# Optimization experiments

Hardware: AMD Instinct MI355X
Metric: run time of the kernel (lower is better)

Reference implementation:

```python
import jax, jax.numpy as jnp
import numpy as np

N_LEVELS = 8
N_FEATS = 8            # features per level
BASE_RES = 16
PER_LEVEL_SCALE = 1.2599210739135742
LOG2_HASHMAP = 19
TABLE_PAD = 8192       # padded per-level table rows (>= max level size 6568)
N_POINTS = 262144


def _level_params(l):
    # tcnn: scale = base * s^l - 1 ; res = ceil(scale)+1 ; size = min(2^19, round_up(res^2, 8))
    scale = BASE_RES * (PER_LEVEL_SCALE ** l) - 1.0
    res = int(np.ceil(scale)) + 1
    size = min(1 << LOG2_HASHMAP, ((res * res + 7) // 8) * 8)
    return float(scale), res, size


def hashgrid_encode(x, table):
    """x: [N,2] in [0,1), table: [L, TABLE_PAD, F]. Returns [N, L*F]."""
    outs = []
    for l in range(N_LEVELS):
        scale, res, size = _level_params(l)
        pos = x * jnp.float32(scale) + jnp.float32(0.5)
        pg = jnp.floor(pos)
        frac = pos - pg
        pg = pg.astype(jnp.int32)
        # Smoothstep interpolation weights: t^2 (3 - 2t)
        w = frac * frac * (3.0 - 2.0 * frac)          # [N,2]
        feat = jnp.zeros((x.shape[0], N_FEATS), dtype=table.dtype)
        for dx in (0, 1):
            wx = w[:, 0] if dx else 1.0 - w[:, 0]
            for dy in (0, 1):
                wy = w[:, 1] if dy else 1.0 - w[:, 1]
                # dense grid index (all levels here fit the hashmap), modulo level size as in tcnn
                idx = ((pg[:, 0] + dx) + (pg[:, 1] + dy) * res) % size
                feat = feat + (wx * wy)[:, None] * table[l, idx]  # irregular gather
        outs.append(feat)
    return jnp.concatenate(outs, axis=-1)  # [N, 64]


def mlp(enc, W0, W1, W2, W3):
    h = jax.nn.relu(enc @ W0)
    h = jax.nn.relu(h @ W1)
    h = jax.nn.relu(h @ W2)
    return h @ W3  # linear output activation


def setup_inputs() -> dict:
    key = jax.random.key(0)
    ks = jax.random.split(key, 6)
    x = jax.random.uniform(ks[0], (N_POINTS, 2), dtype=jnp.float32)
    # tcnn initializes grid params ~ uniform(-1e-4, 1e-4); small values
    table = jax.random.normal(ks[1], (N_LEVELS, TABLE_PAD, N_FEATS), dtype=jnp.float32) * 1e-2
    W0 = jax.random.normal(ks[2], (64, 256), dtype=jnp.float32) * (1.0 / np.sqrt(64))
    W1 = jax.random.normal(ks[3], (256, 256), dtype=jnp.float32) * (1.0 / np.sqrt(256))
    W2 = jax.random.normal(ks[4], (256, 256), dtype=jnp.float32) * (1.0 / np.sqrt(256))
    W3 = jax.random.normal(ks[5], (256, 1), dtype=jnp.float32) * (1.0 / np.sqrt(256))
    return {"x": x, "table": table, "W0": W0, "W1": W1, "W2": W2, "W3": W3}


def reference(x, table, W0, W1, W2, W3):
    enc = hashgrid_encode(x, table)
    return mlp(enc, W0, W1, W2, W3)  # [N, 1]
```

## Files before the change

kernel.cpp:

```cpp
#include <hip/hip_runtime.h>
#include <cmath>


#define N_LEVELS 8
#define TABLE_PAD 8192
#define TILE_M 64
#define ACT_STRIDE 264

typedef __attribute__((ext_vector_type(8))) short short8;
typedef __attribute__((ext_vector_type(16))) float float16v;

struct LevelParams {
  float scale[N_LEVELS];
  int   res[N_LEVELS];
  int   size[N_LEVELS];
};

__device__ __forceinline__ unsigned short f2bf(float f) {
  unsigned int u = __float_as_uint(f);
  u += 0x7fffu + ((u >> 16) & 1u);
  return (unsigned short)(u >> 16);
}
__device__ __forceinline__ unsigned int pack2bf(float a, float b) {
  a = a > 0.f ? a : 0.f;
  b = b > 0.f ? b : 0.f;
  return (unsigned int)f2bf(a) | ((unsigned int)f2bf(b) << 16);
}

__global__ void pack_weights_kernel(const float* __restrict__ W0,
                                    const float* __restrict__ W1,
                                    const float* __restrict__ W2,
                                    unsigned short* __restrict__ Wp) {
  int tid = blockIdx.x * blockDim.x + threadIdx.x;
  const float* src;
  int base, e;
  if (tid < 16384)        { src = W0; base = 0;     e = tid;         }
  else if (tid < 81920)   { src = W1; base = 16384; e = tid - 16384; }
  else if (tid < 147456)  { src = W2; base = 81920; e = tid - 81920; }
  else return;
  int ki = e & 15;
  int n  = (e >> 4) & 255;
  int kb = e >> 12;
  unsigned int u = __float_as_uint(src[(kb * 16 + ki) * 256 + n]);
  u += 0x7fffu + ((u >> 16) & 1u);
  Wp[base + e] = (unsigned short)(u >> 16);
}

__global__ __launch_bounds__(512, 8) void neural_field_kernel(
    const float* __restrict__ x,
    const float* __restrict__ table,
    const unsigned short* __restrict__ Wp,
    const float* __restrict__ W3,
    float* __restrict__ out,
    LevelParams P) {
  __shared__ unsigned short bufA[TILE_M * ACT_STRIDE];
  __shared__ float fsum[TILE_M * 9];

  const int t  = threadIdx.x;
  const int g0 = blockIdx.x * TILE_M;

  const int lane  = t & 63;
  const int w     = t >> 6;
  const int l31   = lane & 31;
  const int h8    = lane >> 5;
  const int wbase = w * 32;

  const int woff = (wbase + l31) * 16 + h8 * 8;

  {
    int p = t & 63;
    int l = t >> 6;
    float2 xy = ((const float2*)x)[g0 + p];
    float scale = P.scale[l];
    int res = P.res[l], size = P.size[l];
    float posx = xy.x * scale + 0.5f;
    float posy = xy.y * scale + 0.5f;
    float pgx = floorf(posx), pgy = floorf(posy);
    float fx = posx - pgx, fy = posy - pgy;
    float wx = fx * fx * (3.0f - 2.0f * fx);
    float wy = fy * fy * (3.0f - 2.0f * fy);
    int px = (int)pgx, py = (int)pgy;
    float acc[8] = {0, 0, 0, 0, 0, 0, 0, 0};
    for (int dy = 0; dy < 2; ++dy) {
      float wyv = dy ? wy : 1.0f - wy;
      for (int dx = 0; dx < 2; ++dx) {
        float wgt = (dx ? wx : 1.0f - wx) * wyv;
        int idx = (px + dx) + (py + dy) * res;
        if (idx >= size) idx -= size;
        const float4* tp =
            (const float4*)(table + ((size_t)l * TABLE_PAD + idx) * 8);
        float4 t0 = tp[0], t1 = tp[1];
        acc[0] += wgt * t0.x; acc[1] += wgt * t0.y;
        acc[2] += wgt * t0.z; acc[3] += wgt * t0.w;
        acc[4] += wgt * t1.x; acc[5] += wgt * t1.y;
        acc[6] += wgt * t1.z; acc[7] += wgt * t1.w;
      }
    }
    union { unsigned short s[8]; short8 v; } u;
    for (int j = 0; j < 8; ++j) u.s[j] = f2bf(acc[j]);
    *(short8*)&bufA[p * ACT_STRIDE + l * 8] = u.v;
  }

  auto run_layer = [&](const unsigned short* Wpl, int KB, short8 wf0,
                       bool inplace, bool fuse_final) {
    float16v acc[2];
#pragma unroll
    for (int j = 0; j < 16; ++j) { acc[0][j] = 0.f; acc[1][j] = 0.f; }

    const unsigned short* ap0 = &bufA[l31 * ACT_STRIDE + h8 * 8];
    const unsigned short* ap1 = ap0 + 32 * ACT_STRIDE;
    const unsigned short* wp  = Wpl + woff;

    short8 af0[2];
    af0[0] = *(const short8*)(ap0);
    af0[1] = *(const short8*)(ap1);

#pragma unroll
    for (int kb = 0; kb < KB; ++kb) {
      short8 wf1, af1[2];
      int kn = (kb + 1 < KB) ? kb + 1 : kb;
      wf1    = *(const short8*)(wp + kn * 4096);
      af1[0] = *(const short8*)(ap0 + kn * 16);
      af1[1] = *(const short8*)(ap1 + kn * 16);

      acc[0] = __builtin_amdgcn_mfma_f32_32x32x16_bf16(wf0, af0[0], acc[0],
                                                       0, 0, 0);
      acc[1] = __builtin_amdgcn_mfma_f32_32x32x16_bf16(wf0, af0[1], acc[1],
                                                       0, 0, 0);
      wf0 = wf1; af0[0] = af1[0]; af0[1] = af1[1];
    }

    if (inplace) __syncthreads();

    if (!fuse_final) {
#pragma unroll
      for (int pt = 0; pt < 2; ++pt) {
        int m = pt * 32 + l31;
#pragma unroll
        for (int q = 0; q < 4; ++q) {
          int n0 = wbase + 8 * q + 4 * h8;
          uint2 pk;
          pk.x = pack2bf(acc[pt][4 * q + 0], acc[pt][4 * q + 1]);
          pk.y = pack2bf(acc[pt][4 * q + 2], acc[pt][4 * q + 3]);
          *(uint2*)&bufA[m * ACT_STRIDE + n0] = pk;
        }
      }
    } else {
      float part0 = 0.f, part1 = 0.f;
#pragma unroll
      for (int q = 0; q < 4; ++q) {
        float4 wv = *(const float4*)(W3 + wbase + 8 * q + 4 * h8);
        float w3v[4] = {wv.x, wv.y, wv.z, wv.w};
#pragma unroll
        for (int r = 0; r < 4; ++r) {
          float v0 = acc[0][4 * q + r]; v0 = v0 > 0.f ? v0 : 0.f;
          float v1 = acc[1][4 * q + r]; v1 = v1 > 0.f ? v1 : 0.f;
          part0 += v0 * w3v[r];
          part1 += v1 * w3v[r];
        }
      }
      part0 += __shfl_xor(part0, 32);
      part1 += __shfl_xor(part1, 32);
      float val = h8 ? part1 : part0;
      fsum[lane * 9 + w] = val;
    }
  };

  short8 wf = *(const short8*)(Wp + woff);
  __syncthreads();
  run_layer(Wp, 4, wf, true, false);
  wf = *(const short8*)(Wp + 16384 + woff);
  __syncthreads();
  run_layer(Wp + 16384, 16, wf, true, false);
  wf = *(const short8*)(Wp + 81920 + woff);
  __syncthreads();
  run_layer(Wp + 81920, 16, wf, false, true);
  __syncthreads();

  {
    int p = t >> 3;
    int q = t & 7;
    float v = fsum[p * 9 + q];
    v += __shfl_xor(v, 1);
    v += __shfl_xor(v, 2);
    v += __shfl_xor(v, 4);
    if (q == 0) out[g0 + p] = v;
  }
}

extern "C" void kernel_launch(void* const* d_in, const int* in_sizes, int n_in,
                              void* d_out, int out_size, void* d_ws,
                              size_t ws_size, hipStream_t stream) {
  const float* x     = (const float*)d_in[0];
  const float* table = (const float*)d_in[1];
  const float* W0    = (const float*)d_in[2];
  const float* W1    = (const float*)d_in[3];
  const float* W2    = (const float*)d_in[4];
  const float* W3    = (const float*)d_in[5];
  float* out = (float*)d_out;
  int N = in_sizes[0] / 2;

  unsigned short* Wp = (unsigned short*)d_ws;

  LevelParams P;
  const double c = 1.2599210739135742;
  double m = 1.0;
  for (int l = 0; l < N_LEVELS; ++l) {
    double scale_d = 16.0 * m - 1.0;
    int res = (int)std::ceil(scale_d) + 1;
    long long sz = ((long long)res * res + 7) / 8 * 8;
    if (sz > (1LL << 19)) sz = 1LL << 19;
    P.scale[l] = (float)scale_d;
    P.res[l]   = res;
    P.size[l]  = (int)sz;
    m *= c;
  }

  hipLaunchKernelGGL(pack_weights_kernel, dim3(576), dim3(256), 0, stream,
                     W0, W1, W2, Wp);
  hipLaunchKernelGGL(neural_field_kernel, dim3(N / TILE_M), dim3(512), 0,
                     stream, x, table, Wp, W3, out, P);
}
```

Measured before the change: 167.9 us.

## Replace syncthreads with lighter barriers and prefetch next layer weights

Swaps __syncthreads for explicit s_waitcnt lgkmcnt(0) plus s_barrier with compiler fences, so the barriers stop waiting on outstanding global memory loads. Issues the first weight fragment load before the hash-grid encode, and each layer's final iteration prefetches the next layer's first weight fragment so global latency overlaps compute. Also peels the last K iteration and lowers launch_bounds min blocks from 8 to 6, which gives the compiler more registers per thread. Manual waitcnt handling is fragile, and a missing wait could expose race hazards.

```diff
diff --git a/kernel.cpp b/kernel.cpp
--- a/kernel.cpp
+++ b/kernel.cpp
@@ -9,6 +9,9 @@
 
 typedef __attribute__((ext_vector_type(8))) short short8;
 typedef __attribute__((ext_vector_type(16))) float float16v;
+
+#define LGKM0() asm volatile("s_waitcnt lgkmcnt(0)" ::: "memory")
+#define CFENCE() asm volatile("" ::: "memory")
 
 struct LevelParams {
   float scale[N_LEVELS];
@@ -46,7 +49,7 @@
   Wp[base + e] = (unsigned short)(u >> 16);
 }
 
-__global__ __launch_bounds__(512, 8) void neural_field_kernel(
+__global__ __launch_bounds__(512, 6) void neural_field_kernel(
     const float* __restrict__ x,
     const float* __restrict__ table,
     const unsigned short* __restrict__ Wp,
@@ -66,6 +69,8 @@
   const int wbase = w * 32;
 
   const int woff = (wbase + l31) * 16 + h8 * 8;
+
+  short8 wf = *(const short8*)(Wp + woff);
 
   {
     int p = t & 63;
@@ -101,8 +106,13 @@
     *(short8*)&bufA[p * ACT_STRIDE + l * 8] = u.v;
   }
 
+  LGKM0();
+  __builtin_amdgcn_s_barrier();
+  CFENCE();
+
   auto run_layer = [&](const unsigned short* Wpl, int KB, short8 wf0,
-                       bool inplace, bool fuse_final) {
+                       bool inplace, bool fuse_final,
+                       const unsigned short* WpNext) -> short8 {
     float16v acc[2];
 #pragma unroll
     for (int j = 0; j < 16; ++j) { acc[0][j] = 0.f; acc[1][j] = 0.f; }
@@ -111,26 +121,31 @@
     const unsigned short* ap1 = ap0 + 32 * ACT_STRIDE;
     const unsigned short* wp  = Wpl + woff;
 
-    short8 af0[2];
-    af0[0] = *(const short8*)(ap0);
-    af0[1] = *(const short8*)(ap1);
-
-#pragma unroll
-    for (int kb = 0; kb < KB; ++kb) {
-      short8 wf1, af1[2];
-      int kn = (kb + 1 < KB) ? kb + 1 : kb;
-      wf1    = *(const short8*)(wp + kn * 4096);
-      af1[0] = *(const short8*)(ap0 + kn * 16);
-      af1[1] = *(const short8*)(ap1 + kn * 16);
-
-      acc[0] = __builtin_amdgcn_mfma_f32_32x32x16_bf16(wf0, af0[0], acc[0],
+    short8 a0 = *(const short8*)(ap0);
+    short8 a1 = *(const short8*)(ap1);
+
+#pragma unroll
+    for (int kb = 0; kb < KB - 1; ++kb) {
+      short8 wn = *(const short8*)(wp + (kb + 1) * 4096);
+      short8 b0 = *(const short8*)(ap0 + (kb + 1) * 16);
+      short8 b1 = *(const short8*)(ap1 + (kb + 1) * 16);
+      acc[0] = __builtin_amdgcn_mfma_f32_32x32x16_bf16(wf0, a0, acc[0],
                                                        0, 0, 0);
-      acc[1] = __builtin_amdgcn_mfma_f32_32x32x16_bf16(wf0, af0[1], acc[1],
+      acc[1] = __builtin_amdgcn_mfma_f32_32x32x16_bf16(wf0, a1, acc[1],
                                                        0, 0, 0);
-      wf0 = wf1; af0[0] = af1[0]; af0[1] = af1[1];
-    }
-
-    if (inplace) __syncthreads();
+      wf0 = wn; a0 = b0; a1 = b1;
+    }
+    short8 wnext{};
+    if (WpNext) wnext = *(const short8*)(WpNext + woff);
+    acc[0] = __builtin_amdgcn_mfma_f32_32x32x16_bf16(wf0, a0, acc[0],
+                                                     0, 0, 0);
+    acc[1] = __builtin_amdgcn_mfma_f32_32x32x16_bf16(wf0, a1, acc[1],
+                                                     0, 0, 0);
+
+    if (inplace) {
+      __builtin_amdgcn_s_barrier();
+      CFENCE();
+    }
 
     if (!fuse_final) {
 #pragma unroll
@@ -164,18 +179,21 @@
       float val = h8 ? part1 : part0;
       fsum[lane * 9 + w] = val;
     }
+    return wnext;
   };
 
-  short8 wf = *(const short8*)(Wp + woff);
-  __syncthreads();
-  run_layer(Wp, 4, wf, true, false);
-  wf = *(const short8*)(Wp + 16384 + woff);
-  __syncthreads();
-  run_layer(Wp + 16384, 16, wf, true, false);
-  wf = *(const short8*)(Wp + 81920 + woff);
-  __syncthreads();
-  run_layer(Wp + 81920, 16, wf, false, true);
-  __syncthreads();
+  wf = run_layer(Wp, 4, wf, true, false, Wp + 16384);
+  LGKM0();
+  __builtin_amdgcn_s_barrier();
+  CFENCE();
+  wf = run_layer(Wp + 16384, 16, wf, true, false, Wp + 81920);
+  LGKM0();
+  __builtin_amdgcn_s_barrier();
+  CFENCE();
+  run_layer(Wp + 81920, 16, wf, false, true, nullptr);
+  LGKM0();
+  __builtin_amdgcn_s_barrier();
+  CFENCE();
 
   {
     int p = t >> 3;
```

Result: faster. 162.8 us (-3.0%).
